# Performance work log

Hardware: AMD Instinct MI355X
Metric: run time of the kernel (lower is better)

## Reference

```python
import jax, jax.numpy as jnp
import numpy as np

ROUTING_ITERS = 3
EPS = 1e-9


def coord_addition(votes):
    # votes: (B, H, W, C, O, 16). Add scaled (row, col) center coords to
    # elements 3 (col/width) and 7 (row/height) of the vote matrix.
    B, H, W, C, O, D = votes.shape
    w_off = (jnp.arange(W, dtype=votes.dtype) + 0.5) / W  # (W,)
    h_off = (jnp.arange(H, dtype=votes.dtype) + 0.5) / H  # (H,)
    off = jnp.zeros((H, W, D), dtype=votes.dtype)
    off = off.at[:, :, 3].add(w_off[None, :])
    off = off.at[:, :, 7].add(h_off[:, None])
    return votes + off[None, :, :, None, None, :]


def em_routing(votes, act, beta_a, beta_u):
    # votes: (B, N, O, 16); act: (B, N, 1); beta_a/beta_u: (1, 1, O, 1)
    B, N, O, D = votes.shape
    rr = jnp.full((B, N, O, 1), 1.0 / O, dtype=votes.dtype)
    act = act[..., None]  # (B, N, 1, 1)
    it_min, it_max = 1.0, min(float(ROUTING_ITERS), 3.0)
    for it in range(ROUTING_ITERS):
        inv_temp = it_min + (it_max - it_min) * it / max(1.0, ROUTING_ITERS - 1)
        # ---- M-step: weighted Gaussian fit per parent capsule ----
        rr_p = rr * act                                     # (B, N, O, 1)
        rr_sum = jnp.sum(rr_p, axis=1, keepdims=True) + EPS  # (B, 1, O, 1)
        mu = jnp.sum(rr_p * votes, axis=1, keepdims=True) / rr_sum     # (B,1,O,16)
        var = jnp.sum(rr_p * (votes - mu) ** 2, axis=1, keepdims=True) / rr_sum + EPS
        cost_h = (beta_u + 0.5 * jnp.log(var)) * rr_sum      # (B, 1, O, 16)
        act_out = jax.nn.sigmoid(
            inv_temp * (beta_a - jnp.sum(cost_h, axis=-1, keepdims=True)))  # (B,1,O,1)
        # ---- E-step: update routing assignments (skip on last iter) ----
        if it < ROUTING_ITERS - 1:
            ln_p = -0.5 * jnp.sum(
                (votes - mu) ** 2 / var + jnp.log(2.0 * jnp.pi * var),
                axis=-1, keepdims=True)                      # (B, N, O, 1)
            rr = jax.nn.softmax(jnp.log(act_out + EPS) + ln_p, axis=2)
    pose_out = mu[:, 0]          # (B, O, 16)
    act_out = act_out[:, 0, :, 0]  # (B, O)
    return pose_out, act_out


def setup_inputs() -> dict:
    key = jax.random.key(0)
    k1, k2, k3, k4, k5 = jax.random.split(key, 5)
    B, H, W, C, O = 64, 14, 14, 32, 10
    pose_in = jax.random.normal(k1, (B, H, W, C, 16), dtype=jnp.float32)
    activation_in = jax.random.uniform(k2, (B, H, W, C, 1), dtype=jnp.float32)
    w = jax.random.truncated_normal(k3, -2.0, 2.0, (C, O, 4, 4), dtype=jnp.float32)
    beta_a = jax.random.normal(k4, (1, 1, O, 1), dtype=jnp.float32)
    beta_u = jax.random.normal(k5, (1, 1, O, 1), dtype=jnp.float32)
    return {"pose_in": pose_in, "activation_in": activation_in, "w": w,
            "beta_a": beta_a, "beta_u": beta_u}


def reference(pose_in, activation_in, w, beta_a, beta_u):
    B, H, W, C, _ = pose_in.shape
    O = w.shape[1]
    # Vote computation: many small 4x4 matmuls, weights shared across positions.
    pose = pose_in.reshape(B, H, W, C, 4, 4)
    votes = jnp.einsum('bhwcij,cojk->bhwcoik', pose, w)  # (B,H,W,C,O,4,4)
    votes = votes.reshape(B, H, W, C, O, 16)
    votes = coord_addition(votes)
    votes_flat = votes.reshape(B, H * W * C, O, 16)
    act_flat = activation_in.reshape(B, H * W * C, 1)
    pose_out, activation_out = em_routing(votes_flat, act_flat, beta_a, beta_u)
    return pose_out, activation_out
```

## Files before the change

kernel.cpp:

```cpp
#include <hip/hip_runtime.h>
#include <hip/hip_bf16.h>

#define BB 64
#define NN 6272
#define OO 10
#define TPB 320
#define EPSF 1e-9f
#define LOG2E 1.44269504f
#define HLOG2E 0.72134752f

#define EXP2F(x) __builtin_amdgcn_exp2f(x)
#define RCPF(x)  __builtin_amdgcn_rcpf(x)

#define ACC_PER_IT 21120
#define OFF_ACC 0
#define OFF_GPART 63360

__device__ __forceinline__ void lds_barrier() {
    asm volatile("s_waitcnt lgkmcnt(0)" ::: "memory");
    __builtin_amdgcn_s_barrier();
    asm volatile("" ::: "memory");
}

__global__ __launch_bounds__(TPB, 3) void fc_moments(
    const float* __restrict__ pose, const float* __restrict__ actv,
    float* __restrict__ gpart)
{
    __shared__ float smem0[5 * 2208];

    const int t = threadIdx.x;
    const int lane = t & 63;
    const int wv = t >> 6;
    const int c = lane & 31;
    const int slot = t >> 5;
    const int chunk = blockIdx.x;
    const int b = blockIdx.y;

    float A1[16], M[40], Vw[4], Vh[4];
    float S0 = 0.f, Uw = 0.f, Uh = 0.f, sw2 = 0.f, sh2 = 0.f;
    #pragma unroll
    for (int k = 0; k < 16; k++) A1[k] = 0.f;
    #pragma unroll
    for (int k = 0; k < 40; k++) M[k] = 0.f;
    #pragma unroll
    for (int k = 0; k < 4; k++) { Vw[k] = 0.f; Vh[k] = 0.f; }

    float4 n0, n1, n2, n3; float na;
    {
        const int hw = chunk * 28 + slot;
        const size_t row = (size_t)b * NN + (hw << 5) + c;
        const float4* p = (const float4*)(pose + row * 16);
        n0 = p[0]; n1 = p[1]; n2 = p[2]; n3 = p[3];
        na = actv[row];
    }

    for (int r = 0; r < 3; r++) {
        const int hl = slot + 10 * r;
        if (hl >= 28) break;

        const float4 q0 = n0, q1 = n1, q2 = n2, q3 = n3;
        const float aq = na;

        const int hln = hl + 10;
        if (hln < 28) {
            const int hwn = chunk * 28 + hln;
            const size_t rown = (size_t)b * NN + (hwn << 5) + c;
            const float4* p = (const float4*)(pose + rown * 16);
            n0 = p[0]; n1 = p[1]; n2 = p[2]; n3 = p[3];
            na = actv[rown];
        }

        const int hw = chunk * 28 + hl;
        const int hi = hw / 14;
        const int wi = hw - hi * 14;
        const float offw = (wi + 0.5f) * (1.0f / 14.0f);
        const float offh = (hi + 0.5f) * (1.0f / 14.0f);

        const float ra = 0.1f * aq;
        const float raw = ra * offw, rah = ra * offh;
        S0 += ra; Uw += raw; Uh += rah;
        sw2 = fmaf(raw, offw, sw2); sh2 = fmaf(rah, offh, sh2);

        #define FOLD_I(qq, i)                                              \
        {                                                                  \
            const float x = qq.x, y = qq.y, z = qq.z, w = qq.w;            \
            const float t0 = ra * x, t1 = ra * y, t2 = ra * z, t3 = ra * w;\
            A1[i*4+0] += t0; A1[i*4+1] += t1;                              \
            A1[i*4+2] += t2; A1[i*4+3] += t3;                              \
            M[i*10+0] = fmaf(t0, x, M[i*10+0]);                            \
            M[i*10+1] = fmaf(t0, y, M[i*10+1]);                            \
            M[i*10+2] = fmaf(t0, z, M[i*10+2]);                            \
            M[i*10+3] = fmaf(t0, w, M[i*10+3]);                            \
            M[i*10+4] = fmaf(t1, y, M[i*10+4]);                            \
            M[i*10+5] = fmaf(t1, z, M[i*10+5]);                            \
            M[i*10+6] = fmaf(t1, w, M[i*10+6]);                            \
            M[i*10+7] = fmaf(t2, z, M[i*10+7]);                            \
            M[i*10+8] = fmaf(t2, w, M[i*10+8]);                            \
            M[i*10+9] = fmaf(t3, w, M[i*10+9]);                            \
        }
        FOLD_I(q0, 0) FOLD_I(q1, 1) FOLD_I(q2, 2) FOLD_I(q3, 3)
        #undef FOLD_I
        Vw[0] = fmaf(raw, q0.x, Vw[0]); Vw[1] = fmaf(raw, q0.y, Vw[1]);
        Vw[2] = fmaf(raw, q0.z, Vw[2]); Vw[3] = fmaf(raw, q0.w, Vw[3]);
        Vh[0] = fmaf(rah, q1.x, Vh[0]); Vh[1] = fmaf(rah, q1.y, Vh[1]);
        Vh[2] = fmaf(rah, q1.z, Vh[2]); Vh[3] = fmaf(rah, q1.w, Vh[3]);
    }

    float* myrow = &smem0[wv * 2208 + c * 69];
    #define FOLDW(arr, n, base)                                            \
    _Pragma("unroll")                                                      \
    for (int k2 = 0; k2 < n; k2++) {                                       \
        float x = arr[k2] + __shfl_xor(arr[k2], 32, 64);                   \
        if (lane < 32) myrow[base + k2] = x;                               \
    }
    FOLDW(A1, 16, 0) FOLDW(M, 40, 16) FOLDW(Vw, 4, 56) FOLDW(Vh, 4, 60)
    #undef FOLDW
    {
        float x0 = S0 + __shfl_xor(S0, 32, 64);
        float x1 = Uw + __shfl_xor(Uw, 32, 64);
        float x2 = Uh + __shfl_xor(Uh, 32, 64);
        float x3 = sw2 + __shfl_xor(sw2, 32, 64);
        float x4 = sh2 + __shfl_xor(sh2, 32, 64);
        if (lane < 32) {
            myrow[64] = x0; myrow[65] = x1; myrow[66] = x2;
            myrow[67] = x3; myrow[68] = x4;
        }
    }
    __syncthreads();
    float* gb = gpart + ((size_t)b * 7 + chunk) * 2208;
    for (int e = t; e < 2208; e += TPB) {
        gb[e] = smem0[e] + smem0[2208 + e] + smem0[2*2208 + e]
              + smem0[3*2208 + e] + smem0[4*2208 + e];
    }
}

__global__ __launch_bounds__(TPB) void fc_transform(
    const float* __restrict__ gpart, const float* __restrict__ wgt,
    float* __restrict__ acc)
{
    __shared__ float smem0[2208];
    const int t = threadIdx.x;
    const int b = blockIdx.x;

    {
        float* z1 = acc + ACC_PER_IT + (size_t)b * OO * 33;
        float* z2 = acc + 2 * ACC_PER_IT + (size_t)b * OO * 33;
        for (int e = t; e < 330; e += TPB) { z1[e] = 0.f; z2[e] = 0.f; }
    }

    const float* gb = gpart + (size_t)b * 7 * 2208;
    for (int e = t; e < 2208; e += TPB) {
        float s = 0.f;
        #pragma unroll
        for (int ch = 0; ch < 7; ch++) s += gb[ch * 2208 + e];
        smem0[e] = s;
    }
    __syncthreads();

    const int oo = t >> 5, k = t & 31;
    float* ab = acc + ((size_t)b * OO + oo) * 33;
    if (k < 16) {
        const int i = k >> 2, kk = k & 3;
        float s = 0.f, s0acc = 0.f;
        #pragma unroll 4
        for (int cc = 0; cc < 32; cc++) {
            const float* mc = &smem0[cc * 69];
            const float* wc = wgt + cc * 160 + oo * 16 + kk;
            const float w0 = wc[0], w1 = wc[4], w2 = wc[8], w3 = wc[12];
            s += w0*mc[i*4+0] + w1*mc[i*4+1] + w2*mc[i*4+2] + w3*mc[i*4+3];
            if (k == 3) s += mc[65];
            if (k == 7) s += mc[66];
            if (k == 0) s0acc += mc[64];
        }
        ab[k] = s;
        if (k == 0) ab[32] = s0acc;
    } else {
        const int km = k - 16, i = km >> 2, kk = km & 3;
        float s = 0.f;
        #pragma unroll 4
        for (int cc = 0; cc < 32; cc++) {
            const float* mc = &smem0[cc * 69];
            const float* mi = mc + 16 + i * 10;
            const float* wc = wgt + cc * 160 + oo * 16 + kk;
            const float w0 = wc[0], w1 = wc[4], w2 = wc[8], w3 = wc[12];
            float q = w0*(w0*mi[0] + 2.f*(w1*mi[1] + w2*mi[2] + w3*mi[3]))
                    + w1*(w1*mi[4] + 2.f*(w2*mi[5] + w3*mi[6]))
                    + w2*(w2*mi[7] + 2.f*w3*mi[8])
                    + w3*(w3*mi[9]);
            s += q;
            if (km == 3) s += 2.f*(w0*mc[56]+w1*mc[57]+w2*mc[58]+w3*mc[59]) + mc[67];
            if (km == 7) s += 2.f*(w0*mc[60]+w1*mc[61]+w2*mc[62]+w3*mc[63]) + mc[68];
        }
        ab[k] = s;
    }
}

__global__ __launch_bounds__(256) void fc_pass(
    const float* __restrict__ pose, const float* __restrict__ actv,
    const float* __restrict__ wgt,
    const float* __restrict__ accPrev,
    const float* __restrict__ beta_a, const float* __restrict__ beta_u,
    float* __restrict__ accOut, float inv_temp)
{
    __shared__ float smem[256 * 17];
    __shared__ float ivL[10 * 36];
    __shared__ float m2L[10 * 36];
    __shared__ float bL[12];

    const int t = threadIdx.x;
    const int lane = t & 63;
    const int w4 = t >> 6;
    const int nl = lane / 10;
    const int o = lane - nl * 10;
    const bool lanereal = (nl < 6);
    const int gbase = (lanereal ? nl : 0) * 10;

    const int bx = blockIdx.x;
    const int chunk = bx >> 3;
    const int c = ((bx & 7) << 2) + w4;
    const int b = blockIdx.y;

    const int hwbase = chunk * 98;
    const size_t rowbase = (size_t)b * NN + ((size_t)hwbase << 5) + c;

    float wr[16];
    {
        const float4* wp = (const float4*)(wgt + ((c * OO + o) << 4));
        float4 a0 = wp[0], a1 = wp[1], a2 = wp[2], a3 = wp[3];
        wr[0]=a0.x; wr[1]=a0.y; wr[2]=a0.z; wr[3]=a0.w;
        wr[4]=a1.x; wr[5]=a1.y; wr[6]=a1.z; wr[7]=a1.w;
        wr[8]=a2.x; wr[9]=a2.y; wr[10]=a2.z; wr[11]=a2.w;
        wr[12]=a3.x; wr[13]=a3.y; wr[14]=a3.z; wr[15]=a3.w;
    }

    if (t < 10) {
        const float* ab = accPrev + ((size_t)b * OO + t) * 33;
        const float S0p = ab[32];
        const float rs = S0p + EPSF;
        const float rsi = RCPF(rs);
        float sv = 0.f, csum = 0.f;
        #pragma unroll
        for (int d = 0; d < 16; d++) {
            const float s1 = ab[d], s2 = ab[16 + d];
            const float m = s1 * rsi;
            float vraw = fmaf(m * m, S0p, fmaf(-2.f * m, s1, s2));
            vraw = fmaxf(vraw, 0.f);
            const float var = fmaf(vraw, rsi, EPSF);
            sv += __logf(var);
            const float ivd = RCPF(var);
            const float i2 = ivd * HLOG2E;
            ivL[t * 36 + d] = i2;
            m2L[t * 36 + d] = 2.f * m * i2;
            csum = fmaf(m * m, i2, csum);
        }
        const float cost = rs * fmaf(0.5f, sv, 16.f * beta_u[t]);
        const float act = RCPF(1.f + __expf(-inv_temp * (beta_a[t] - cost)));
        const float biasN = __logf(act + EPSF) - 0.5f * sv;
        const float biasL = biasN * LOG2E;
        bL[t] = biasL - csum;
        float ub = biasL;
        #pragma unroll
        for (int j = 0; j < OO; j++) ub = fmaxf(ub, __shfl(biasL, j, 64));
        if (t == 0) bL[10] = ub - 64.f;
    }
    lds_barrier();

    float iv2[16], m2iv[16];
    {
        const float4* ip = (const float4*)&ivL[o * 36];
        float4 x0 = ip[0], x1 = ip[1], x2 = ip[2], x3 = ip[3];
        iv2[0]=x0.x; iv2[1]=x0.y; iv2[2]=x0.z; iv2[3]=x0.w;
        iv2[4]=x1.x; iv2[5]=x1.y; iv2[6]=x1.z; iv2[7]=x1.w;
        iv2[8]=x2.x; iv2[9]=x2.y; iv2[10]=x2.z; iv2[11]=x2.w;
        iv2[12]=x3.x; iv2[13]=x3.y; iv2[14]=x3.z; iv2[15]=x3.w;
        const float4* mp = (const float4*)&m2L[o * 36];
        float4 y0 = mp[0], y1 = mp[1], y2 = mp[2], y3 = mp[3];
        m2iv[0]=y0.x; m2iv[1]=y0.y; m2iv[2]=y0.z; m2iv[3]=y0.w;
        m2iv[4]=y1.x; m2iv[5]=y1.y; m2iv[6]=y1.z; m2iv[7]=y1.w;
        m2iv[8]=y2.x; m2iv[9]=y2.y; m2iv[10]=y2.z; m2iv[11]=y2.w;
        m2iv[12]=y3.x; m2iv[13]=y3.y; m2iv[14]=y3.z; m2iv[15]=y3.w;
    }
    const float bias2 = bL[o];
    const float UBs = bL[10];

    float S1[16], S2[16], S0 = 0.f;
    #pragma unroll
    for (int d = 0; d < 16; d++) { S1[d] = 0.f; S2[d] = 0.f; }

    for (int step = 0; step < 17; ++step) {
        const int hl = step * 6 + nl;
        const bool valid = lanereal && (hl < 98);
        const int hle = valid ? hl : 0;
        const int hw = hwbase + hle;
        const size_t row = rowbase + ((size_t)hle << 5);

        const float4* pp = (const float4*)(pose + row * 16);
        float4 q0 = pp[0], q1 = pp[1], q2 = pp[2], q3 = pp[3];
        const float a = valid ? actv[row] : 0.f;

        const int hq = hw / 14;
        const float offw = ((hw - hq * 14) + 0.5f) * (1.0f / 14.0f);
        const float offh = (hq + 0.5f) * (1.0f / 14.0f);

        float p[16];
        p[0]=q0.x; p[1]=q0.y; p[2]=q0.z; p[3]=q0.w;
        p[4]=q1.x; p[5]=q1.y; p[6]=q1.z; p[7]=q1.w;
        p[8]=q2.x; p[9]=q2.y; p[10]=q2.z; p[11]=q2.w;
        p[12]=q3.x; p[13]=q3.y; p[14]=q3.z; p[15]=q3.w;

        float v[16];
        #pragma unroll
        for (int ii = 0; ii < 4; ii++) {
            #pragma unroll
            for (int kk = 0; kk < 4; kk++) {
                float vv = fmaf(p[ii*4+0], wr[0*4+kk],
                           fmaf(p[ii*4+1], wr[1*4+kk],
                           fmaf(p[ii*4+2], wr[2*4+kk],
                                p[ii*4+3] * wr[3*4+kk])));
                if (ii == 0 && kk == 3) vv += offw;
                if (ii == 1 && kk == 3) vv += offh;
                v[ii*4+kk] = vv;
            }
        }

        float pa = 0.f, pb = 0.f, pc = 0.f, pd = 0.f;
        #pragma unroll
        for (int ii = 0; ii < 4; ii++) {
            float t0 = fmaf(-v[ii*4+0], iv2[ii*4+0], m2iv[ii*4+0]);
            float t1 = fmaf(-v[ii*4+1], iv2[ii*4+1], m2iv[ii*4+1]);
            float t2 = fmaf(-v[ii*4+2], iv2[ii*4+2], m2iv[ii*4+2]);
            float t3 = fmaf(-v[ii*4+3], iv2[ii*4+3], m2iv[ii*4+3]);
            pa = fmaf(v[ii*4+0], t0, pa);
            pb = fmaf(v[ii*4+1], t1, pb);
            pc = fmaf(v[ii*4+2], t2, pc);
            pd = fmaf(v[ii*4+3], t3, pd);
        }
        const float lg = bias2 + ((pa + pb) + (pc + pd));

        const float ef = EXP2F(lg - UBs);
        float efs[OO];
        #pragma unroll
        for (int j = 0; j < OO; j++) efs[j] = __shfl(ef, gbase + j, 64);
        float s01 = efs[0]+efs[1], s23 = efs[2]+efs[3], s45 = efs[4]+efs[5];
        float s67 = efs[6]+efs[7], s89 = efs[8]+efs[9];
        const float sum = (((s01+s23) + (s45+s67)) + s89) + 1e-30f;
        const float rr = ef * (a * RCPF(sum));

        #pragma unroll
        for (int d = 0; d < 16; d++) {
            const float rv = rr * v[d];
            S1[d] += rv;
            S2[d] = fmaf(rv, v[d], S2[d]);
        }
        S0 += rr;
    }

    float* accB = accOut + (size_t)b * OO * 33;
    #pragma unroll
    for (int k = 0; k < 16; k++) smem[t * 17 + k] = S1[k];
    smem[t * 17 + 16] = S0;
    __syncthreads();
    for (int u = t; u < 170; u += 256) {
        const int oo = u / 17, kk = u - 17 * oo;
        float s = 0.f;
        #pragma unroll
        for (int wq = 0; wq < 4; wq++) {
            #pragma unroll
            for (int nn = 0; nn < 6; nn++)
                s += smem[(wq * 64 + nn * 10 + oo) * 17 + kk];
        }
        atomicAdd(accB + oo * 33 + ((kk < 16) ? kk : 32), s);
    }
    __syncthreads();
    #pragma unroll
    for (int k = 0; k < 16; k++) smem[t * 17 + k] = S2[k];
    __syncthreads();
    for (int u = t; u < 160; u += 256) {
        const int oo = u >> 4, kk = u & 15;
        float s = 0.f;
        #pragma unroll
        for (int wq = 0; wq < 4; wq++) {
            #pragma unroll
            for (int nn = 0; nn < 6; nn++)
                s += smem[(wq * 64 + nn * 10 + oo) * 17 + kk];
        }
        atomicAdd(accB + oo * 33 + 16 + kk, s);
    }
}

__global__ __launch_bounds__(256) void fc_stats(
    const float* __restrict__ acc, const float* __restrict__ beta_a,
    const float* __restrict__ beta_u,
    float* __restrict__ out, float inv_temp)
{
    const int t = threadIdx.x;
    const int b = blockIdx.x;
    if (t >= 160) return;
    const int o = t >> 4, d = t & 15;
    const float* ab = acc + ((size_t)b * OO + o) * 33;
    const float S1 = ab[d], S2 = ab[16 + d], S0 = ab[32];
    const float rs = S0 + EPSF;
    const float mu = S1 / rs;
    float vraw = fmaf(mu * mu, S0, fmaf(-2.f * mu, S1, S2));
    vraw = fmaxf(vraw, 0.f);
    const float var = vraw / rs + EPSF;
    const float lv = __logf(var);
    float sv = lv;
    #pragma unroll
    for (int off = 8; off >= 1; off >>= 1) sv += __shfl_xor(sv, off, 16);
    const float cost = rs * fmaf(0.5f, sv, 16.f * beta_u[o]);
    const float av = 1.f / (1.f + __expf(-inv_temp * (beta_a[o] - cost)));
    out[((size_t)b * OO + o) * 16 + d] = mu;
    if (d == 0) out[BB * OO * 16 + b * OO + o] = av;
}

extern "C" void kernel_launch(void* const* d_in, const int* in_sizes, int n_in,
                              void* d_out, int out_size, void* d_ws, size_t ws_size,
                              hipStream_t stream) {
    const float* pose   = (const float*)d_in[0];
    const float* actv   = (const float*)d_in[1];
    const float* wgt    = (const float*)d_in[2];
    const float* beta_a = (const float*)d_in[3];
    const float* beta_u = (const float*)d_in[4];
    float* out = (float*)d_out;
    float* ws  = (float*)d_ws;

    float* acc0  = ws + OFF_ACC;
    float* acc1  = ws + OFF_ACC + ACC_PER_IT;
    float* acc2  = ws + OFF_ACC + 2 * ACC_PER_IT;
    float* gpart = ws + OFF_GPART;

    fc_moments<<<dim3(7, BB), dim3(TPB), 0, stream>>>(pose, actv, gpart);
    fc_transform<<<BB, dim3(TPB), 0, stream>>>(gpart, wgt, acc0);
    fc_pass<<<dim3(16, BB), dim3(256), 0, stream>>>(pose, actv, wgt, acc0, beta_a, beta_u, acc1, 1.0f);
    fc_pass<<<dim3(16, BB), dim3(256), 0, stream>>>(pose, actv, wgt, acc1, beta_a, beta_u, acc2, 2.0f);
    fc_stats<<<BB, 256, 0, stream>>>(acc2, beta_a, beta_u, out, 3.0f);
}
```

Baseline: 163.8 us.

## Stage weights in LDS and halve per-block work to double fc_pass grid

Each wave now writes its 4x4 weight matrices into shared memory once, and lanes read them back as float4 inside the vote loop instead of holding 16 weight registers. This is meant to cut register pressure and raise occupancy. The per-block spatial chunk drops from 98 to 49 positions and the grid grows from 16 to 32 blocks per batch, giving more parallelism but doubling the atomicAdd reductions. The shared buffer is reused for the reduction, so a barrier is added after the loop to protect it.

```diff
diff --git a/kernel.cpp b/kernel.cpp
--- a/kernel.cpp
+++ b/kernel.cpp
@@ -203,9 +203,10 @@
     float* __restrict__ accOut, float inv_temp)
 {
     __shared__ float smem[256 * 17];
-    __shared__ float ivL[10 * 36];
-    __shared__ float m2L[10 * 36];
-    __shared__ float bL[12];
+    float* wrL = smem;
+    float* ivL = smem + 800;
+    float* m2L = smem + 1160;
+    float* bL  = smem + 1520;
 
     const int t = threadIdx.x;
     const int lane = t & 63;
@@ -220,17 +221,17 @@
     const int c = ((bx & 7) << 2) + w4;
     const int b = blockIdx.y;
 
-    const int hwbase = chunk * 98;
+    const int hwbase = chunk * 49;
     const size_t rowbase = (size_t)b * NN + ((size_t)hwbase << 5) + c;
 
-    float wr[16];
-    {
+    if (nl == 0) {
         const float4* wp = (const float4*)(wgt + ((c * OO + o) << 4));
         float4 a0 = wp[0], a1 = wp[1], a2 = wp[2], a3 = wp[3];
-        wr[0]=a0.x; wr[1]=a0.y; wr[2]=a0.z; wr[3]=a0.w;
-        wr[4]=a1.x; wr[5]=a1.y; wr[6]=a1.z; wr[7]=a1.w;
-        wr[8]=a2.x; wr[9]=a2.y; wr[10]=a2.z; wr[11]=a2.w;
-        wr[12]=a3.x; wr[13]=a3.y; wr[14]=a3.z; wr[15]=a3.w;
+        float* dst = &wrL[(w4 * 10 + o) * 20];
+        *(float4*)(dst + 0)  = a0;
+        *(float4*)(dst + 4)  = a1;
+        *(float4*)(dst + 8)  = a2;
+        *(float4*)(dst + 12) = a3;
     }
 
     if (t < 10) {
@@ -282,14 +283,15 @@
     }
     const float bias2 = bL[o];
     const float UBs = bL[10];
+    const float* wrow = &wrL[(w4 * 10 + o) * 20];
 
     float S1[16], S2[16], S0 = 0.f;
     #pragma unroll
     for (int d = 0; d < 16; d++) { S1[d] = 0.f; S2[d] = 0.f; }
 
-    for (int step = 0; step < 17; ++step) {
+    for (int step = 0; step < 9; ++step) {
         const int hl = step * 6 + nl;
-        const bool valid = lanereal && (hl < 98);
+        const bool valid = lanereal && (hl < 49);
         const int hle = valid ? hl : 0;
         const int hw = hwbase + hle;
         const size_t row = rowbase + ((size_t)hle << 5);
@@ -310,16 +312,17 @@
 
         float v[16];
         #pragma unroll
-        for (int ii = 0; ii < 4; ii++) {
+        for (int k2 = 0; k2 < 16; k2++) v[k2] = 0.f;
+        v[3] = offw; v[7] = offh;
+        #pragma unroll
+        for (int dd = 0; dd < 4; dd++) {
+            const float4 wf = *(const float4*)(wrow + dd * 4);
             #pragma unroll
-            for (int kk = 0; kk < 4; kk++) {
-                float vv = fmaf(p[ii*4+0], wr[0*4+kk],
-                           fmaf(p[ii*4+1], wr[1*4+kk],
-                           fmaf(p[ii*4+2], wr[2*4+kk],
-                                p[ii*4+3] * wr[3*4+kk])));
-                if (ii == 0 && kk == 3) vv += offw;
-                if (ii == 1 && kk == 3) vv += offh;
-                v[ii*4+kk] = vv;
+            for (int ii = 0; ii < 4; ii++) {
+                v[ii*4+0] = fmaf(p[ii*4+dd], wf.x, v[ii*4+0]);
+                v[ii*4+1] = fmaf(p[ii*4+dd], wf.y, v[ii*4+1]);
+                v[ii*4+2] = fmaf(p[ii*4+dd], wf.z, v[ii*4+2]);
+                v[ii*4+3] = fmaf(p[ii*4+dd], wf.w, v[ii*4+3]);
             }
         }
 
@@ -355,6 +358,7 @@
         S0 += rr;
     }
 
+    lds_barrier();
     float* accB = accOut + (size_t)b * OO * 33;
     #pragma unroll
     for (int k = 0; k < 16; k++) smem[t * 17 + k] = S1[k];
@@ -432,7 +436,7 @@
 
     fc_moments<<<dim3(7, BB), dim3(TPB), 0, stream>>>(pose, actv, gpart);
     fc_transform<<<BB, dim3(TPB), 0, stream>>>(gpart, wgt, acc0);
-    fc_pass<<<dim3(16, BB), dim3(256), 0, stream>>>(pose, actv, wgt, acc0, beta_a, beta_u, acc1, 1.0f);
-    fc_pass<<<dim3(16, BB), dim3(256), 0, stream>>>(pose, actv, wgt, acc1, beta_a, beta_u, acc2, 2.0f);
+    fc_pass<<<dim3(32, BB), dim3(256), 0, stream>>>(pose, actv, wgt, acc0, beta_a, beta_u, acc1, 1.0f);
+    fc_pass<<<dim3(32, BB), dim3(256), 0, stream>>>(pose, actv, wgt, acc1, beta_a, beta_u, acc2, 2.0f);
     fc_stats<<<BB, 256, 0, stream>>>(acc2, beta_a, beta_u, out, 3.0f);
 }
```

Result: slower. 171.0 us (+4.4%).
